# Performance work log

Hardware: AMD Instinct MI355X
Metric: run time of the kernel (lower is better)

The kernel has to match this reference:

```python
import jax, jax.numpy as jnp
import numpy as np

D_MODEL = 512
N_HEADS = 8
HEAD_DIM = D_MODEL // N_HEADS


def setup_inputs() -> dict:
    key = jax.random.key(0)
    ks = jax.random.split(key, 7)
    x = jax.random.normal(ks[0], (8, 2048, D_MODEL), dtype=jnp.float32)
    ln_gamma = jnp.ones((D_MODEL,), jnp.float32)
    ln_beta = jnp.zeros((D_MODEL,), jnp.float32)
    s = 1.0 / np.sqrt(D_MODEL)
    W_qkv = jax.random.uniform(ks[1], (3 * D_MODEL, D_MODEL), jnp.float32, -s, s)
    b_qkv = jax.random.uniform(ks[2], (3 * D_MODEL,), jnp.float32, -s, s)
    W_out = jax.random.uniform(ks[3], (D_MODEL, D_MODEL), jnp.float32, -s, s)
    b_out = jax.random.uniform(ks[4], (D_MODEL,), jnp.float32, -s, s)
    return {"x": x, "ln_gamma": ln_gamma, "ln_beta": ln_beta,
            "W_qkv": W_qkv, "b_qkv": b_qkv, "W_out": W_out, "b_out": b_out}


def reference(x, ln_gamma, ln_beta, W_qkv, b_qkv, W_out, b_out):
    b, s, d = x.shape
    # LayerNorm (eps=1e-5, torch default)
    mu = jnp.mean(x, axis=-1, keepdims=True)
    var = jnp.mean(jnp.square(x - mu), axis=-1, keepdims=True)
    xn = (x - mu) * jax.lax.rsqrt(var + 1e-5) * ln_gamma + ln_beta
    # QKV projection (torch Linear: x @ W.T + b)
    qkv = xn @ W_qkv.T + b_qkv                       # [b, s, 3d]
    qkv = qkv.reshape(b, s, 3, N_HEADS, HEAD_DIM)
    qkv = jnp.transpose(qkv, (2, 0, 3, 1, 4))        # [3, b, h, s, hd]
    q, k, v = qkv[0], qkv[1], qkv[2]
    scale = HEAD_DIM ** -0.5
    attn = jnp.einsum('bhqd,bhkd->bhqk', q, k) * scale
    attn = jax.nn.softmax(attn, axis=-1)
    out = jnp.einsum('bhqk,bhkd->bhqd', attn, v)     # [b, h, s, hd]
    out = jnp.transpose(out, (0, 2, 1, 3)).reshape(b, s, d)
    return out @ W_out.T + b_out
```

## Files before the change

kernel.cpp:

```cpp
#include <hip/hip_runtime.h>
#include <stdint.h>

#define NH 8
#define HD 64
#define BATCH 8
#define SEQ 2048
#define DM 512
#define TOK (BATCH * SEQ)

#define QSCALE 0.18033688011112042f

typedef __attribute__((ext_vector_type(8))) __bf16 bf16x8;
typedef __attribute__((ext_vector_type(4))) float f32x4;
typedef __attribute__((ext_vector_type(16))) float f32x16;
typedef __attribute__((ext_vector_type(8))) uint16_t u16x8;

__device__ __forceinline__ uint16_t f2bf(float f) {
  union { __bf16 h; uint16_t u; } c;
  c.h = (__bf16)f;
  return c.u;
}

__device__ __forceinline__ void load_lds16(const void* g, void* l) {
  __builtin_amdgcn_global_load_lds(
      (const __attribute__((address_space(1))) void*)g,
      (__attribute__((address_space(3))) void*)l, 16, 0, 0);
}

#define VM_DRAIN() asm volatile("s_waitcnt vmcnt(0)" ::: "memory")

__device__ __forceinline__ int swz128(int row, int kbyte) {
  return (row * 128 + kbyte) ^ ((row & 7) << 4);
}

#define MFMA16(a, b, c) __builtin_amdgcn_mfma_f32_16x16x32_bf16(a, b, c, 0, 0, 0)
#define MFMA32(a, b, c) __builtin_amdgcn_mfma_f32_32x32x16_bf16(a, b, c, 0, 0, 0)

__global__ __launch_bounds__(256) void ln_kernel(
    const float* __restrict__ x, const float* __restrict__ gam,
    const float* __restrict__ bet, uint16_t* __restrict__ xn) {
  const int row = blockIdx.x * 4 + (threadIdx.x >> 6);
  const int lane = threadIdx.x & 63;
  const float4* xr = (const float4*)(x + (size_t)row * DM);
  float4 a0 = xr[lane * 2 + 0];
  float4 a1 = xr[lane * 2 + 1];
  float s = a0.x + a0.y + a0.z + a0.w + a1.x + a1.y + a1.z + a1.w;
  float q = a0.x * a0.x + a0.y * a0.y + a0.z * a0.z + a0.w * a0.w +
            a1.x * a1.x + a1.y * a1.y + a1.z * a1.z + a1.w * a1.w;
#pragma unroll
  for (int m = 1; m < 64; m <<= 1) {
    s += __shfl_xor(s, m);
    q += __shfl_xor(q, m);
  }
  const float mean = s * (1.0f / DM);
  const float var = q * (1.0f / DM) - mean * mean;
  const float rstd = rsqrtf(var + 1e-5f);
  const float4* gv = (const float4*)gam;
  const float4* bv = (const float4*)bet;
  float4 g0 = gv[lane * 2], g1 = gv[lane * 2 + 1];
  float4 b0 = bv[lane * 2], b1 = bv[lane * 2 + 1];
  u16x8 r;
  r[0] = f2bf((a0.x - mean) * rstd * g0.x + b0.x);
  r[1] = f2bf((a0.y - mean) * rstd * g0.y + b0.y);
  r[2] = f2bf((a0.z - mean) * rstd * g0.z + b0.z);
  r[3] = f2bf((a0.w - mean) * rstd * g0.w + b0.w);
  r[4] = f2bf((a1.x - mean) * rstd * g1.x + b1.x);
  r[5] = f2bf((a1.y - mean) * rstd * g1.y + b1.y);
  r[6] = f2bf((a1.z - mean) * rstd * g1.z + b1.z);
  r[7] = f2bf((a1.w - mean) * rstd * g1.w + b1.w);
  *(u16x8*)(xn + (size_t)row * DM + lane * 8) = r;
}

__global__ __launch_bounds__(256) void cast_w(const float* __restrict__ w,
                                              uint16_t* __restrict__ o, int n8) {
  int i = blockIdx.x * 256 + threadIdx.x;
  if (i >= n8) return;
  const float4* p = (const float4*)w + (size_t)i * 2;
  float4 a0 = p[0], a1 = p[1];
  u16x8 r;
  r[0] = f2bf(a0.x); r[1] = f2bf(a0.y); r[2] = f2bf(a0.z); r[3] = f2bf(a0.w);
  r[4] = f2bf(a1.x); r[5] = f2bf(a1.y); r[6] = f2bf(a1.z); r[7] = f2bf(a1.w);
  *(u16x8*)(o + (size_t)i * 8) = r;
}

template <int EPI>
__global__ __launch_bounds__(256) void gemm_nt(
    const uint16_t* __restrict__ A, const uint16_t* __restrict__ Bw,
    const float* __restrict__ bias, uint16_t* __restrict__ oq,
    uint16_t* __restrict__ okk, uint16_t* __restrict__ ov,
    float* __restrict__ oc) {
  __shared__ __align__(16) char As[128 * 64 * 2];
  __shared__ __align__(16) char Bs[128 * 64 * 2];
  const int tid = threadIdx.x;
  const int lane = tid & 63;
  const int w = tid >> 6;
  const int wr = (w >> 1) * 64;
  const int wc = (w & 1) * 64;
  const int l15 = lane & 15;
  const int l4 = lane >> 4;
  const size_t tileM = (size_t)blockIdx.y * 128;
  const int tileN = blockIdx.x * 128;
  const int trow = tid >> 3;
  const int tcol = tid & 7;
  const f32x4 vzero = {0.f, 0.f, 0.f, 0.f};

  f32x4 acc[4][4];
#pragma unroll
  for (int m = 0; m < 4; ++m)
#pragma unroll
    for (int n = 0; n < 4; ++n) acc[m][n] = vzero;

  for (int kt = 0; kt < 8; ++kt) {
    if (kt) __syncthreads();
#pragma unroll
    for (int i = 0; i < 4; ++i) {
      const int row = i * 32 + trow;
      const int c0 = 8 * (tcol ^ (row & 7));
      load_lds16(A + (tileM + row) * DM + kt * 64 + c0, As + i * 4096 + w * 1024);
      load_lds16(Bw + (size_t)(tileN + row) * DM + kt * 64 + c0, Bs + i * 4096 + w * 1024);
    }
    VM_DRAIN();
    __syncthreads();
#pragma unroll
    for (int ks = 0; ks < 2; ++ks) {
      const int kb = ks * 64 + l4 * 16;
      bf16x8 af[4], bfr[4];
#pragma unroll
      for (int m = 0; m < 4; ++m) {
        const int r = wr + m * 16 + l15;
        af[m] = *(const bf16x8*)(As + swz128(r, kb));
      }
#pragma unroll
      for (int n = 0; n < 4; ++n) {
        const int r = wc + n * 16 + l15;
        bfr[n] = *(const bf16x8*)(Bs + swz128(r, kb));
      }
#pragma unroll
      for (int m = 0; m < 4; ++m)
#pragma unroll
        for (int n = 0; n < 4; ++n)
          acc[m][n] = MFMA16(af[m], bfr[n], acc[m][n]);
    }
  }

#pragma unroll
  for (int m = 0; m < 4; ++m) {
    const size_t row0 = tileM + wr + m * 16 + l4 * 4;
#pragma unroll
    for (int n = 0; n < 4; ++n) {
      const int col = tileN + wc + n * 16 + l15;
      const float bb = bias[col];
#pragma unroll
      for (int jj = 0; jj < 4; ++jj) {
        const float val = acc[m][n][jj] + bb;
        const size_t r = row0 + jj;
        if (EPI == 0) {
          const int wh = col >> 9;
          const int rem = col & 511;
          const int h = rem >> 6;
          const int dd = rem & 63;
          const int bi = (int)(r >> 11);
          const int si = (int)(r & 2047);
          const size_t bh = (size_t)bi * NH + h;
          if (wh == 0)
            oq[(bh * SEQ + si) * HD + dd] = f2bf(val * QSCALE);
          else if (wh == 1)
            okk[(bh * SEQ + si) * HD + dd] = f2bf(val);
          else
            ov[(bh * HD + dd) * SEQ + si] = f2bf(val);
        } else {
          oc[r * DM + col] = val;
        }
      }
    }
  }
}

__global__ __launch_bounds__(256, 3) void attn_kernel(
    const uint16_t* __restrict__ qb, const uint16_t* __restrict__ kb,
    const uint16_t* __restrict__ vb, uint16_t* __restrict__ ab) {
  __shared__ __align__(16) char Ks[2 * 64 * 128];
  __shared__ __align__(16) char Vs[2 * 64 * 128];
  __shared__ float corrbuf[4 * 32];
  const int tid = threadIdx.x;
  const int lane = tid & 63;
  const int wq = tid >> 6;
  const int l31 = lane & 31;
  const int h = lane >> 5;
  const int bh = blockIdx.x >> 4;
  const int qt = blockIdx.x & 15;
  const uint16_t* qp = qb + (size_t)bh * SEQ * HD;
  const uint16_t* kp = kb + (size_t)bh * SEQ * HD;
  const uint16_t* vp = vb + (size_t)bh * HD * SEQ;
  const int trow = tid >> 3;
  const int tcol = tid & 7;

  auto stageK = [&](int tt, char* dst) {
    const int kv0 = tt * 64;
#pragma unroll
    for (int i = 0; i < 2; ++i) {
      const int row = i * 32 + trow;
      const int c0 = 8 * (tcol ^ (row & 7));
      load_lds16(kp + (size_t)(kv0 + row) * HD + c0, dst + i * 4096 + wq * 1024);
    }
  };
  auto stageV = [&](int tt, char* dst) {
    const int kv0 = tt * 64;
#pragma unroll
    for (int i = 0; i < 2; ++i) {
      const int row = i * 32 + trow;
      const int c0 = 8 * (tcol ^ (row & 7));
      load_lds16(vp + (size_t)row * SEQ + kv0 + c0, dst + i * 4096 + wq * 1024);
    }
  };

  bf16x8 qf[4];
  const int q0 = qt * 128 + wq * 32;
#pragma unroll
  for (int c = 0; c < 4; ++c)
    qf[c] = *(const bf16x8*)(qp + (size_t)(q0 + l31) * HD + c * 16 + h * 8);

  f32x16 oacc0, oacc1;
#pragma unroll
  for (int r = 0; r < 16; ++r) { oacc0[r] = 0.f; oacc1[r] = 0.f; }
  float mrow = -1e30f;
  float lsum = 0.f;

  auto build2 = [&](const f32x16& s, float m, bf16x8* fa, bf16x8* fb, float& rs) {
    uint32_t u[8];
#pragma unroll
    for (int i2 = 0; i2 < 8; ++i2) {
      float plo = exp2f(s[2 * i2] - m);
      float phi = exp2f(s[2 * i2 + 1] - m);
      rs += plo + phi;
      asm("v_cvt_pk_bf16_f32 %0, %1, %2" : "=v"(u[i2]) : "v"(plo), "v"(phi));
    }
    asm("v_permlane32_swap_b32 %0, %1" : "+v"(u[0]), "+v"(u[2]));
    asm("v_permlane32_swap_b32 %0, %1" : "+v"(u[1]), "+v"(u[3]));
    asm("v_permlane32_swap_b32 %0, %1" : "+v"(u[4]), "+v"(u[6]));
    asm("v_permlane32_swap_b32 %0, %1" : "+v"(u[5]), "+v"(u[7]));
    union { uint32_t w[4]; bf16x8 v; } A, B;
    A.w[0] = u[0]; A.w[1] = u[1]; A.w[2] = u[2]; A.w[3] = u[3];
    B.w[0] = u[4]; B.w[1] = u[5]; B.w[2] = u[6]; B.w[3] = u[7];
    *fa = A.v; *fb = B.v;
  };

  auto tile = [&](const char* Kc, const char* Vc) {
    f32x16 s0, s1;
#pragma unroll
    for (int r = 0; r < 16; ++r) { s0[r] = 0.f; s1[r] = 0.f; }
#pragma unroll
    for (int c = 0; c < 4; ++c) {
      const int kbyte = c * 32 + h * 16;
      bf16x8 kf0 = *(const bf16x8*)(Kc + swz128(l31, kbyte));
      bf16x8 kf1 = *(const bf16x8*)(Kc + swz128(32 + l31, kbyte));
      s0 = MFMA32(kf0, qf[c], s0);
      s1 = MFMA32(kf1, qf[c], s1);
    }

    float r8[8];
#pragma unroll
    for (int i = 0; i < 8; ++i)
      r8[i] = fmaxf(fmaxf(s0[2 * i], s0[2 * i + 1]), fmaxf(s1[2 * i], s1[2 * i + 1]));
    float mx = fmaxf(fmaxf(fmaxf(r8[0], r8[1]), fmaxf(r8[2], r8[3])),
                     fmaxf(fmaxf(r8[4], r8[5]), fmaxf(r8[6], r8[7])));
    mx = fmaxf(mx, __shfl_xor(mx, 32));
    const float mold = mrow;
    const float mnew = fmaxf(mold, mx);
    const float corr = exp2f(mold - mnew);
    mrow = mnew;

    corrbuf[wq * 32 + l31] = corr;
    float4 cg[4];
#pragma unroll
    for (int g = 0; g < 4; ++g)
      cg[g] = *(const float4*)(corrbuf + wq * 32 + 8 * g + 4 * h);
#pragma unroll
    for (int rg = 0; rg < 4; ++rg)
#pragma unroll
      for (int rj = 0; rj < 4; ++rj) {
        const float cc = cg[rg][rj];
        const int r = rg * 4 + rj;
        oacc0[r] *= cc; oacc1[r] *= cc;
      }

    float rs = 0.f;
    bf16x8 pa[4];
    build2(s0, mrow, &pa[0], &pa[1], rs);
    build2(s1, mrow, &pa[2], &pa[3], rs);
    rs += __shfl_xor(rs, 32);
    lsum = lsum * corr + rs;

#pragma unroll
    for (int i = 0; i < 4; ++i) {
      const int kbyte = i * 32 + h * 16;
      bf16x8 v0 = *(const bf16x8*)(Vc + swz128(l31, kbyte));
      bf16x8 v1 = *(const bf16x8*)(Vc + swz128(32 + l31, kbyte));
      oacc0 = MFMA32(pa[i], v0, oacc0);
      oacc1 = MFMA32(pa[i], v1, oacc1);
    }
  };

  char* K0 = Ks;        char* V0 = Vs;
  char* K1 = Ks + 8192; char* V1 = Vs + 8192;

  stageK(0, K0);
  stageV(0, V0);
  VM_DRAIN();
  __syncthreads();

  for (int t = 0; t < SEQ / 64; t += 2) {
    stageK(t + 1, K1);
    stageV(t + 1, V1);
    tile(K0, V0);
    VM_DRAIN();
    __syncthreads();

    if (t + 2 < SEQ / 64) {
      stageK(t + 2, K0);
      stageV(t + 2, V0);
    }
    tile(K1, V1);
    VM_DRAIN();
    __syncthreads();
  }

  corrbuf[wq * 32 + l31] = lsum;
  __builtin_amdgcn_s_waitcnt(0);

  const int bi = bh >> 3;
  const int head = bh & 7;
#pragma unroll
  for (int r = 0; r < 16; ++r) {
    const int q = (r & 3) + 8 * (r >> 2) + 4 * h;
    const float inv = 1.0f / corrbuf[wq * 32 + q];
    const size_t tok = (size_t)bi * SEQ + qt * 128 + wq * 32 + q;
    ab[tok * DM + head * HD + l31] = f2bf(oacc0[r] * inv);
    ab[tok * DM + head * HD + 32 + l31] = f2bf(oacc1[r] * inv);
  }
}

extern "C" void kernel_launch(void* const* d_in, const int* in_sizes, int n_in,
                              void* d_out, int out_size, void* d_ws, size_t ws_size,
                              hipStream_t stream) {
  const float* x = (const float*)d_in[0];
  const float* gam = (const float*)d_in[1];
  const float* bet = (const float*)d_in[2];
  const float* wqkv = (const float*)d_in[3];
  const float* bqkv = (const float*)d_in[4];
  const float* wout = (const float*)d_in[5];
  const float* bout = (const float*)d_in[6];

  const size_t SZ_XN = (size_t)TOK * DM * 2;
  const size_t SZ_WQ = (size_t)3 * DM * DM * 2;
  const size_t SZ_WO = (size_t)DM * DM * 2;
  const size_t SZ_HDBUF = (size_t)BATCH * NH * SEQ * HD * 2;

  char* p = (char*)d_ws;
  uint16_t* xn = (uint16_t*)p;      p += SZ_XN;
  uint16_t* wq = (uint16_t*)p;      p += SZ_WQ;
  uint16_t* wo = (uint16_t*)p;      p += SZ_WO;
  uint16_t* qbuf = (uint16_t*)p;    p += SZ_HDBUF;
  uint16_t* kbuf = (uint16_t*)p;    p += SZ_HDBUF;
  uint16_t* vbuf = (uint16_t*)p;    p += SZ_HDBUF;
  uint16_t* abuf = xn;

  ln_kernel<<<dim3(TOK / 4), dim3(256), 0, stream>>>(x, gam, bet, xn);
  cast_w<<<dim3((3 * DM * DM / 8) / 256), dim3(256), 0, stream>>>(wqkv, wq, 3 * DM * DM / 8);
  cast_w<<<dim3((DM * DM / 8) / 256), dim3(256), 0, stream>>>(wout, wo, DM * DM / 8);
  gemm_nt<0><<<dim3(12, 128), dim3(256), 0, stream>>>(xn, wq, bqkv, qbuf, kbuf, vbuf, nullptr);
  attn_kernel<<<dim3(BATCH * NH * (SEQ / 128)), dim3(256), 0, stream>>>(qbuf, kbuf, vbuf, abuf);
  gemm_nt<1><<<dim3(4, 128), dim3(256), 0, stream>>>(abuf, wo, bout, nullptr, nullptr, nullptr,
                                                     (float*)d_out);
}
```

Measured before the change: 212.4 us.

## Load K/V fragments directly from global memory in attention, dropping LDS staging

Removes the double-buffered LDS staging of K and V tiles, along with the async global-to-LDS loads and the per-tile barriers. Each wave now reads its K and V MFMA fragments straight from global memory, relying on L1/L2 caching because the four waves in a block share the same K/V. The launch-bounds occupancy hint is also dropped. The risk is exposed global-load latency with no explicit prefetch, plus redundant traffic across waves, in exchange for no synchronisation and less LDS use.

```diff
diff --git a/kernel.cpp b/kernel.cpp
--- a/kernel.cpp
+++ b/kernel.cpp
@@ -176,11 +176,9 @@
   }
 }
 
-__global__ __launch_bounds__(256, 3) void attn_kernel(
+__global__ __launch_bounds__(256) void attn_kernel(
     const uint16_t* __restrict__ qb, const uint16_t* __restrict__ kb,
     const uint16_t* __restrict__ vb, uint16_t* __restrict__ ab) {
-  __shared__ __align__(16) char Ks[2 * 64 * 128];
-  __shared__ __align__(16) char Vs[2 * 64 * 128];
   __shared__ float corrbuf[4 * 32];
   const int tid = threadIdx.x;
   const int lane = tid & 63;
@@ -192,27 +190,9 @@
   const uint16_t* qp = qb + (size_t)bh * SEQ * HD;
   const uint16_t* kp = kb + (size_t)bh * SEQ * HD;
   const uint16_t* vp = vb + (size_t)bh * HD * SEQ;
-  const int trow = tid >> 3;
-  const int tcol = tid & 7;
-
-  auto stageK = [&](int tt, char* dst) {
-    const int kv0 = tt * 64;
-#pragma unroll
-    for (int i = 0; i < 2; ++i) {
-      const int row = i * 32 + trow;
-      const int c0 = 8 * (tcol ^ (row & 7));
-      load_lds16(kp + (size_t)(kv0 + row) * HD + c0, dst + i * 4096 + wq * 1024);
-    }
-  };
-  auto stageV = [&](int tt, char* dst) {
-    const int kv0 = tt * 64;
-#pragma unroll
-    for (int i = 0; i < 2; ++i) {
-      const int row = i * 32 + trow;
-      const int c0 = 8 * (tcol ^ (row & 7));
-      load_lds16(vp + (size_t)row * SEQ + kv0 + c0, dst + i * 4096 + wq * 1024);
-    }
-  };
+
+  const uint16_t* kRow = kp + (size_t)l31 * HD + h * 8;
+  const uint16_t* vRow = vp + (size_t)l31 * SEQ + h * 8;
 
   bf16x8 qf[4];
   const int q0 = qt * 128 + wq * 32;
@@ -245,15 +225,16 @@
     *fa = A.v; *fb = B.v;
   };
 
-  auto tile = [&](const char* Kc, const char* Vc) {
+  for (int t = 0; t < SEQ / 64; ++t) {
+    const int kv0 = t * 64;
+
     f32x16 s0, s1;
 #pragma unroll
     for (int r = 0; r < 16; ++r) { s0[r] = 0.f; s1[r] = 0.f; }
 #pragma unroll
     for (int c = 0; c < 4; ++c) {
-      const int kbyte = c * 32 + h * 16;
-      bf16x8 kf0 = *(const bf16x8*)(Kc + swz128(l31, kbyte));
-      bf16x8 kf1 = *(const bf16x8*)(Kc + swz128(32 + l31, kbyte));
+      bf16x8 kf0 = *(const bf16x8*)(kRow + (size_t)kv0 * HD + c * 16);
+      bf16x8 kf1 = *(const bf16x8*)(kRow + (size_t)(kv0 + 32) * HD + c * 16);
       s0 = MFMA32(kf0, qf[c], s0);
       s1 = MFMA32(kf1, qf[c], s1);
     }
@@ -293,36 +274,11 @@
 
 #pragma unroll
     for (int i = 0; i < 4; ++i) {
-      const int kbyte = i * 32 + h * 16;
-      bf16x8 v0 = *(const bf16x8*)(Vc + swz128(l31, kbyte));
-      bf16x8 v1 = *(const bf16x8*)(Vc + swz128(32 + l31, kbyte));
+      bf16x8 v0 = *(const bf16x8*)(vRow + kv0 + i * 16);
+      bf16x8 v1 = *(const bf16x8*)(vRow + (size_t)32 * SEQ + kv0 + i * 16);
       oacc0 = MFMA32(pa[i], v0, oacc0);
       oacc1 = MFMA32(pa[i], v1, oacc1);
     }
-  };
-
-  char* K0 = Ks;        char* V0 = Vs;
-  char* K1 = Ks + 8192; char* V1 = Vs + 8192;
-
-  stageK(0, K0);
-  stageV(0, V0);
-  VM_DRAIN();
-  __syncthreads();
-
-  for (int t = 0; t < SEQ / 64; t += 2) {
-    stageK(t + 1, K1);
-    stageV(t + 1, V1);
-    tile(K0, V0);
-    VM_DRAIN();
-    __syncthreads();
-
-    if (t + 2 < SEQ / 64) {
-      stageK(t + 2, K0);
-      stageV(t + 2, V0);
-    }
-    tile(K1, V1);
-    VM_DRAIN();
-    __syncthreads();
   }
 
   corrbuf[wq * 32 + l31] = lsum;
```

New measurement: 374.2 us. 1.76x slower.
